# Performance work log

Hardware: AMD Instinct MI355X
Metric: run time of the kernel (lower is better)

## Reference

```python
import jax, jax.numpy as jnp
import numpy as np

GN_EPS = 1e-5
G = 8          # SKA groups
SKS3 = 27      # sks**3


def _aff(x, s, b):
    # folded BatchNorm (eval): per-channel scale + shift on NCDHW tensor
    return x * s[None, :, None, None, None] + b[None, :, None, None, None]


def _c1(x, w):
    # 1x1x1 conv as channel GEMM; w: [O, I]
    return jnp.einsum('bcdhw,oc->bodhw', x, w)


def _dw5(x, w):
    # depthwise 5x5x5 conv, pad=2; w: [C, 1, 5, 5, 5]
    return jax.lax.conv_general_dilated(
        x, w, window_strides=(1, 1, 1), padding=[(2, 2)] * 3,
        dimension_numbers=('NCDHW', 'OIDHW', 'NCDHW'),
        feature_group_count=x.shape[1])


def setup_inputs() -> dict:
    key = jax.random.key(0)
    ks = jax.random.split(key, 24)
    B, C, D, H, W = 2, 64, 32, 32, 32

    def n(k, shape, scale=1.0):
        return jax.random.normal(k, shape, jnp.float32) * scale

    def u(k, shape):
        return jax.random.uniform(k, shape, jnp.float32, 0.5, 1.5)

    return {
        'x': n(ks[0], (B, C, D, H, W)),
        'w1': n(ks[1], (32, 64), 64 ** -0.5),
        's1': u(ks[2], (32,)), 'b1': n(ks[3], (32,), 0.1),
        'w2': n(ks[4], (32, 1, 5, 5, 5), 125 ** -0.5),
        's2': u(ks[5], (32,)), 'b2': n(ks[6], (32,), 0.1),
        'w3': n(ks[7], (32, 32), 32 ** -0.5),
        's3': u(ks[8], (32,)), 'b3': n(ks[9], (32,), 0.1),
        'w4': n(ks[10], (216, 32), 32 ** -0.5), 'b4': n(ks[11], (216,), 0.1),
        'gn_g': u(ks[12], (216,)), 'gn_b': n(ks[13], (216,), 0.1),
        'bn_s': u(ks[14], (64,)), 'bn_b': n(ks[15], (64,), 0.1),
        'pw1_w': n(ks[16], (128, 64), 64 ** -0.5),
        'pw1_s': u(ks[17], (128,)), 'pw1_b': n(ks[18], (128,), 0.1),
        'pw2_w': n(ks[19], (64, 128), 128 ** -0.5),
        'pw2_s': u(ks[20], (64,)), 'pw2_b': n(ks[21], (64,), 0.1),
    }


def reference(x, w1, s1, b1, w2, s2, b2, w3, s3, b3, w4, b4,
              gn_g, gn_b, bn_s, bn_b,
              pw1_w, pw1_s, pw1_b, pw2_w, pw2_s, pw2_b):
    B, C, D, H, W = x.shape

    # ---- LKP3D: dynamic kernel generation ----
    a = jax.nn.relu(_aff(_c1(x, w1), s1, b1))          # cv1 + BN + ReLU
    a = _aff(_dw5(a, w2), s2, b2)                      # cv2 (5^3 dw) + BN
    a = jax.nn.relu(_aff(_c1(a, w3), s3, b3))          # cv3 + BN + ReLU
    wk = _c1(a, w4) + b4[None, :, None, None, None]    # cv4: [B,216,D,H,W]
    # GroupNorm: num_groups = dim//groups = 8, channels = 216
    g = wk.reshape(B, G, SKS3, D, H, W)
    mu = g.mean(axis=(2, 3, 4, 5), keepdims=True)
    var = g.var(axis=(2, 3, 4, 5), keepdims=True)
    g = (g - mu) * jax.lax.rsqrt(var + GN_EPS)
    wk = g.reshape(B, G * SKS3, D, H, W) * gn_g[None, :, None, None, None] \
         + gn_b[None, :, None, None, None]
    wk = wk.reshape(B, G, SKS3, D, H, W)               # [B, G, 27, D, H, W]

    # ---- SKA3D: apply dynamic kernels (27 shifted copies, grouped) ----
    offs = [(di, hi, wi) for di in (-1, 0, 1) for hi in (-1, 0, 1) for wi in (-1, 0, 1)]
    patches = jnp.stack(
        [jnp.roll(x, (-di, -hi, -wi), axis=(2, 3, 4)) for di, hi, wi in offs],
        axis=2)                                        # [B, C, 27, D, H, W]
    p = patches.reshape(B, G, C // G, SKS3, D, H, W)
    sk = jnp.einsum('bgckdhw,bgkdhw->bgcdhw', p, wk).reshape(B, C, D, H, W)

    y = _aff(sk, bn_s, bn_b) + x                       # LSConv BN + residual

    # ---- FFN (residual): pw1 + BN + ReLU + pw2 + BN ----
    f = jax.nn.relu(_aff(_c1(y, pw1_w), pw1_s, pw1_b))
    f = _aff(_c1(f, pw2_w), pw2_s, pw2_b)
    return y + f
```

## Files before the change

### kernel.cpp

```cpp
#include <hip/hip_runtime.h>

#define SPAT 32768
#define BATCH 2
#define GN_EPS 1e-5f

__device__ __forceinline__ void fma2(float2& a, const float2& v, float w) {
    a.x = fmaf(v.x, w, a.x); a.y = fmaf(v.y, w, a.y);
}

template <int CIN, int NO, bool RELU, bool AFF>
__global__ __launch_bounds__(256) void k_c1(
    const float* __restrict__ in, const float* __restrict__ w,
    const float* __restrict__ sc, const float* __restrict__ bi,
    float* __restrict__ out, int Cout)
{
    int q = blockIdx.x * 256 + threadIdx.x;
    int o0 = blockIdx.y * NO, b = blockIdx.z;
    const float2* ip = (const float2*)(in + (size_t)b * CIN * SPAT) + q;
    float2 acc[NO];
#pragma unroll
    for (int i = 0; i < NO; ++i) acc[i] = {0.f, 0.f};
#pragma unroll 4
    for (int c = 0; c < CIN; ++c) {
        float2 v = ip[(size_t)c * (SPAT / 2)];
#pragma unroll
        for (int i = 0; i < NO; ++i)
            fma2(acc[i], v, w[(o0 + i) * CIN + c]);
    }
    float2* op = (float2*)(out + (size_t)b * Cout * SPAT) + q;
#pragma unroll
    for (int i = 0; i < NO; ++i) {
        int o = o0 + i;
        float scale = AFF ? sc[o] : 1.f;
        float shift = bi[o];
        float2 r = acc[i];
        r.x = r.x * scale + shift; r.y = r.y * scale + shift;
        if (RELU) { r.x = fmaxf(r.x, 0.f); r.y = fmaxf(r.y, 0.f); }
        op[(size_t)o * (SPAT / 2)] = r;
    }
}

__global__ __launch_bounds__(256) void k_gram(
    const float* __restrict__ a, float* __restrict__ partial)
{
    __shared__ float lds[32 * 257];
    int blk = blockIdx.x, b = blockIdx.z;
    const float* ap = a + (size_t)b * 32 * SPAT + blk * 256;
    for (int i = threadIdx.x; i < 32 * 64; i += 256) {
        int m = i >> 6, p4 = (i & 63) * 4;
        float4 v = *(const float4*)(ap + (size_t)m * SPAT + p4);
        lds[m * 257 + p4 + 0] = v.x; lds[m * 257 + p4 + 1] = v.y;
        lds[m * 257 + p4 + 2] = v.z; lds[m * 257 + p4 + 3] = v.w;
    }
    __syncthreads();
    float* outp = partial + (size_t)(b * 128 + blk) * 1056;
#pragma unroll
    for (int it = 0; it < 4; ++it) {
        int pid = threadIdx.x + it * 256;
        const float* pa = &lds[(pid >> 5) * 257];
        const float* pb = &lds[(pid & 31) * 257];
        float acc = 0.f;
#pragma unroll 8
        for (int p = 0; p < 256; ++p) acc = fmaf(pa[p], pb[p], acc);
        outp[pid] = acc;
    }
    if (threadIdx.x < 32) {
        const float* pa = &lds[threadIdx.x * 257];
        float scc = 0.f;
#pragma unroll 8
        for (int p = 0; p < 256; ++p) scc += pa[p];
        outp[1024 + threadIdx.x] = scc;
    }
}

__global__ __launch_bounds__(512) void k_stats(
    const float* __restrict__ partial, const float* __restrict__ w4,
    const float* __restrict__ b4, float* __restrict__ stats)
{
    __shared__ float G[2 * 1056];
    __shared__ float sred[432], ssred[432];
    for (int e = threadIdx.x; e < 2 * 1056; e += 512) {
        int b = e / 1056, pid = e % 1056;
        float acc = 0.f;
#pragma unroll 8
        for (int blk = 0; blk < 128; ++blk)
            acc += partial[(size_t)(b * 128 + blk) * 1056 + pid];
        G[e] = acc;
    }
    __syncthreads();
    if (threadIdx.x < 432) {
        int t = threadIdx.x;
        int b = t / 216, r = t % 216, g = r / 27, k = r % 27;
        const float* wk = w4 + (g * 27 + k) * 32;
        float wreg[32];
#pragma unroll
        for (int m = 0; m < 32; ++m) wreg[m] = wk[m];
        const float* Gb = &G[b * 1056];
        const float* Sb = &G[b * 1056 + 1024];
        float sk = 0.f, ssk = 0.f;
#pragma unroll
        for (int m = 0; m < 32; ++m) {
            sk = fmaf(wreg[m], Sb[m], sk);
            float dot = 0.f;
#pragma unroll
            for (int mm = 0; mm < 32; ++mm)
                dot = fmaf(wreg[mm], Gb[m * 32 + mm], dot);
            ssk = fmaf(wreg[m], dot, ssk);
        }
        float bb = b4[g * 27 + k];
        float NN = (float)SPAT;
        ssk += 2.f * bb * sk + NN * bb * bb;
        sk  += NN * bb;
        sred[t] = sk; ssred[t] = ssk;
    }
    __syncthreads();
    if (threadIdx.x < 16) {
        int bg = threadIdx.x;
        float s = 0.f, ss = 0.f;
        for (int k = 0; k < 27; ++k) { s += sred[bg * 27 + k]; ss += ssred[bg * 27 + k]; }
        float N27 = 27.f * (float)SPAT;
        float mu = s / N27;
        float var = ss / N27 - mu * mu;
        stats[bg * 2 + 0] = mu;
        stats[bg * 2 + 1] = rsqrtf(var + GN_EPS);
    }
}

__global__ __launch_bounds__(256) void k_ska(
    const float* __restrict__ x, const float* __restrict__ wk,
    const float* __restrict__ stats,
    const float* __restrict__ gn_g, const float* __restrict__ gn_b,
    const float* __restrict__ bn_s, const float* __restrict__ bn_b,
    float* __restrict__ y)
{
    int q = blockIdx.x * 256 + threadIdx.x;
    int s = q * 4;
    int g = blockIdx.y, b = blockIdx.z;
    int bg = b * 8 + g;
    float mu  = stats[bg * 2 + 0];
    float inv = stats[bg * 2 + 1];
    int d = s >> 10, h = (s >> 5) & 31, w0 = s & 31;
    int lane = threadIdx.x & 63;
    int xl_src = (lane & 56) | ((lane + 7) & 7);
    int xr_src = (lane & 56) | ((lane + 1) & 7);
    const float* xg = x + ((size_t)(b * 64 + g * 8)) * SPAT;
    const float* wp = wk + ((size_t)(b * 216 + g * 27)) * SPAT + s;

    float4 acc[8];
    float4 xc[8];
#pragma unroll
    for (int c = 0; c < 8; ++c) acc[c] = {0.f, 0.f, 0.f, 0.f};

#pragma unroll
    for (int kd = 0; kd < 3; ++kd) {
        int zd = (d + kd + 31) & 31;
#pragma unroll
        for (int kh = 0; kh < 3; ++kh) {
            int zh = (h + kh + 31) & 31;
            int kbase = (kd * 3 + kh) * 3;
            float wn[3][4];
#pragma unroll
            for (int kw = 0; kw < 3; ++kw) {
                int kk = kbase + kw;
                float4 wq = *(const float4*)(wp + (size_t)kk * SPAT);
                float A = gn_g[g * 27 + kk] * inv;
                float B = gn_b[g * 27 + kk] - mu * A;
                wn[kw][0] = wq.x * A + B;
                wn[kw][1] = wq.y * A + B;
                wn[kw][2] = wq.z * A + B;
                wn[kw][3] = wq.w * A + B;
            }
            int rowoff = zd * 1024 + zh * 32;
            bool center = (kd == 1) && (kh == 1);
#pragma unroll
            for (int c = 0; c < 8; ++c) {
                float4 m = *(const float4*)(xg + (size_t)c * SPAT + rowoff + w0);
                if (center) xc[c] = m;
                float xl = __shfl(m.w, xl_src, 64);
                float xr = __shfl(m.x, xr_src, 64);
                float win[6] = {xl, m.x, m.y, m.z, m.w, xr};
#pragma unroll
                for (int kw = 0; kw < 3; ++kw) {
                    acc[c].x = fmaf(win[0 + kw], wn[kw][0], acc[c].x);
                    acc[c].y = fmaf(win[1 + kw], wn[kw][1], acc[c].y);
                    acc[c].z = fmaf(win[2 + kw], wn[kw][2], acc[c].z);
                    acc[c].w = fmaf(win[3 + kw], wn[kw][3], acc[c].w);
                }
            }
        }
    }
#pragma unroll
    for (int c = 0; c < 8; ++c) {
        int ch = g * 8 + c;
        float bs = bn_s[ch], bb = bn_b[ch];
        float4 r;
        r.x = acc[c].x * bs + bb + xc[c].x;
        r.y = acc[c].y * bs + bb + xc[c].y;
        r.z = acc[c].z * bs + bb + xc[c].z;
        r.w = acc[c].w * bs + bb + xc[c].w;
        *(float4*)(y + ((size_t)(b * 64 + ch)) * SPAT + s) = r;
    }
}

__global__ __launch_bounds__(256, 4) void k_dw5(
    const float* __restrict__ in, const float* __restrict__ w2,
    const float* __restrict__ s2, const float* __restrict__ b2,
    float* __restrict__ out)
{
    __shared__ float lds[6 * 36 * 40];
    int tid = threadIdx.x;
    int d0 = blockIdx.x * 2;
    int c = blockIdx.y, b = blockIdx.z;
    const float* ip = in + ((size_t)(b * 32 + c)) * SPAT;

    float4 z = {0.f, 0.f, 0.f, 0.f};
    for (int i = tid; i < 6 * 36 * 40 / 4; i += 256)
        ((float4*)lds)[i] = z;
    __syncthreads();
    for (int i = tid; i < 6 * 256; i += 256) {
        int p = i >> 8, rem = i & 255;
        int r = rem >> 3, c4 = (rem & 7) * 4;
        int d = d0 - 2 + p;
        if (d >= 0 && d < 32) {
            float4 v = *(const float4*)(ip + d * 1024 + r * 32 + c4);
            *(float4*)&lds[p * 1440 + (r + 2) * 40 + (c4 + 4)] = v;
        }
    }
    __syncthreads();

    float scl = s2[c], shf = b2[c];
    const float* wt = w2 + c * 125;
#pragma unroll
    for (int k = 0; k < 2; ++k) {
        int j = tid + k * 256;
        int pd = j >> 8, rem = j & 255;
        int hr = rem >> 3, w4i = (rem & 7) * 4;
        float4 acc = {0.f, 0.f, 0.f, 0.f};
#pragma unroll
        for (int kd = 0; kd < 5; ++kd) {
            const float* pl = &lds[(pd + kd) * 1440];
#pragma unroll
            for (int kh = 0; kh < 5; ++kh) {
                const float* row = pl + (hr + kh) * 40 + w4i;
                float4 r0 = *(const float4*)(row);
                float4 r1 = *(const float4*)(row + 4);
                float4 r2 = *(const float4*)(row + 8);
                float win[12] = {r0.x, r0.y, r0.z, r0.w,
                                 r1.x, r1.y, r1.z, r1.w,
                                 r2.x, r2.y, r2.z, r2.w};
#pragma unroll
                for (int kw = 0; kw < 5; ++kw) {
                    float wv = wt[kd * 25 + kh * 5 + kw];
                    acc.x = fmaf(wv, win[2 + 0 + kw], acc.x);
                    acc.y = fmaf(wv, win[2 + 1 + kw], acc.y);
                    acc.z = fmaf(wv, win[2 + 2 + kw], acc.z);
                    acc.w = fmaf(wv, win[2 + 3 + kw], acc.w);
                }
            }
        }
        acc.x = acc.x * scl + shf; acc.y = acc.y * scl + shf;
        acc.z = acc.z * scl + shf; acc.w = acc.w * scl + shf;
        *(float4*)(out + ((size_t)(b * 32 + c)) * SPAT
                   + (d0 + pd) * 1024 + hr * 32 + w4i) = acc;
    }
}

template <int NO>
__global__ __launch_bounds__(256) void k_pw2_out(
    const float* __restrict__ f1, const float* __restrict__ w,
    const float* __restrict__ sc, const float* __restrict__ bi,
    const float* __restrict__ yres, float* __restrict__ out)
{
    int q = blockIdx.x * 256 + threadIdx.x;
    int o0 = blockIdx.y * NO, b = blockIdx.z;
    const float2* ip = (const float2*)(f1 + (size_t)b * 128 * SPAT) + q;
    float2 acc[NO];
#pragma unroll
    for (int i = 0; i < NO; ++i) acc[i] = {0.f, 0.f};
#pragma unroll 4
    for (int c = 0; c < 128; ++c) {
        float2 v = ip[(size_t)c * (SPAT / 2)];
#pragma unroll
        for (int i = 0; i < NO; ++i)
            fma2(acc[i], v, w[(o0 + i) * 128 + c]);
    }
    const float2* yp = (const float2*)(yres + (size_t)b * 64 * SPAT) + q;
    float2* op = (float2*)(out + (size_t)b * 64 * SPAT) + q;
#pragma unroll
    for (int i = 0; i < NO; ++i) {
        int o = o0 + i;
        float scale = sc[o], shift = bi[o];
        float2 yv = yp[(size_t)o * (SPAT / 2)];
        float2 r = acc[i];
        r.x = r.x * scale + shift + yv.x;
        r.y = r.y * scale + shift + yv.y;
        op[(size_t)o * (SPAT / 2)] = r;
    }
}

extern "C" void kernel_launch(void* const* d_in, const int* in_sizes, int n_in,
                              void* d_out, int out_size, void* d_ws, size_t ws_size,
                              hipStream_t stream)
{
    const float* x     = (const float*)d_in[0];
    const float* w1    = (const float*)d_in[1];
    const float* s1    = (const float*)d_in[2];
    const float* b1    = (const float*)d_in[3];
    const float* w2    = (const float*)d_in[4];
    const float* s2    = (const float*)d_in[5];
    const float* b2    = (const float*)d_in[6];
    const float* w3    = (const float*)d_in[7];
    const float* s3    = (const float*)d_in[8];
    const float* b3    = (const float*)d_in[9];
    const float* w4    = (const float*)d_in[10];
    const float* b4    = (const float*)d_in[11];
    const float* gn_g  = (const float*)d_in[12];
    const float* gn_b  = (const float*)d_in[13];
    const float* bn_s  = (const float*)d_in[14];
    const float* bn_b  = (const float*)d_in[15];
    const float* pw1_w = (const float*)d_in[16];
    const float* pw1_s = (const float*)d_in[17];
    const float* pw1_b = (const float*)d_in[18];
    const float* pw2_w = (const float*)d_in[19];
    const float* pw2_s = (const float*)d_in[20];
    const float* pw2_b = (const float*)d_in[21];

    float* ws    = (float*)d_ws;
    float* a1    = ws;
    float* a2    = a1 + (size_t)BATCH * 32 * SPAT;
    float* yb    = ws;
    float* wkb   = ws + (size_t)BATCH * 64 * SPAT;
    float* f1    = wkb;
    float* part  = wkb + (size_t)BATCH * 216 * SPAT;
    float* stats = part + (size_t)256 * 1056;

    dim3 blk(256);
    k_c1<64, 8, true, true><<<dim3(SPAT / 512, 4, BATCH), blk, 0, stream>>>(
        x, w1, s1, b1, a1, 32);
    k_dw5<<<dim3(16, 32, BATCH), blk, 0, stream>>>(a1, w2, s2, b2, a2);
    k_c1<32, 8, true, true><<<dim3(SPAT / 512, 4, BATCH), blk, 0, stream>>>(
        a2, w3, s3, b3, a1, 32);
    k_gram<<<dim3(128, 1, BATCH), blk, 0, stream>>>(a1, part);
    k_stats<<<dim3(1), dim3(512), 0, stream>>>(part, w4, b4, stats);
    k_c1<32, 8, false, false><<<dim3(SPAT / 512, 27, BATCH), blk, 0, stream>>>(
        a1, w4, nullptr, b4, wkb, 216);
    k_ska<<<dim3(SPAT / 1024, 8, BATCH), blk, 0, stream>>>(
        x, wkb, stats, gn_g, gn_b, bn_s, bn_b, yb);
    k_c1<64, 8, true, true><<<dim3(SPAT / 512, 16, BATCH), blk, 0, stream>>>(
        yb, pw1_w, pw1_s, pw1_b, f1, 128);
    k_pw2_out<8><<<dim3(SPAT / 512, 8, BATCH), blk, 0, stream>>>(
        f1, pw2_w, pw2_s, pw2_b, yb, (float*)d_out);
}
```

Baseline: 281.3 us.

## Fuse FFN into one kernel and compute all output channels per thread

```diff
diff --git a/kernel.cpp b/kernel.cpp
--- a/kernel.cpp
+++ b/kernel.cpp
@@ -4,40 +4,99 @@
 #define BATCH 2
 #define GN_EPS 1e-5f
 
-__device__ __forceinline__ void fma2(float2& a, const float2& v, float w) {
-    a.x = fmaf(v.x, w, a.x); a.y = fmaf(v.y, w, a.y);
-}
-
-template <int CIN, int NO, bool RELU, bool AFF>
-__global__ __launch_bounds__(256) void k_c1(
+template <int CIN, int COUT, bool RELU>
+__global__ __launch_bounds__(256) void k_rc1(
     const float* __restrict__ in, const float* __restrict__ w,
     const float* __restrict__ sc, const float* __restrict__ bi,
-    float* __restrict__ out, int Cout)
-{
-    int q = blockIdx.x * 256 + threadIdx.x;
-    int o0 = blockIdx.y * NO, b = blockIdx.z;
-    const float2* ip = (const float2*)(in + (size_t)b * CIN * SPAT) + q;
-    float2 acc[NO];
-#pragma unroll
-    for (int i = 0; i < NO; ++i) acc[i] = {0.f, 0.f};
+    float* __restrict__ out)
+{
+    int pos = blockIdx.x * 256 + threadIdx.x;
+    int b = blockIdx.z;
+    const float* ip = in + (size_t)b * CIN * SPAT + pos;
+    float acc[COUT];
+#pragma unroll
+    for (int o = 0; o < COUT; ++o) acc[o] = 0.f;
 #pragma unroll 4
     for (int c = 0; c < CIN; ++c) {
-        float2 v = ip[(size_t)c * (SPAT / 2)];
-#pragma unroll
-        for (int i = 0; i < NO; ++i)
-            fma2(acc[i], v, w[(o0 + i) * CIN + c]);
-    }
-    float2* op = (float2*)(out + (size_t)b * Cout * SPAT) + q;
-#pragma unroll
-    for (int i = 0; i < NO; ++i) {
-        int o = o0 + i;
-        float scale = AFF ? sc[o] : 1.f;
-        float shift = bi[o];
-        float2 r = acc[i];
-        r.x = r.x * scale + shift; r.y = r.y * scale + shift;
-        if (RELU) { r.x = fmaxf(r.x, 0.f); r.y = fmaxf(r.y, 0.f); }
-        op[(size_t)o * (SPAT / 2)] = r;
-    }
+        float v = ip[(size_t)c * SPAT];
+#pragma unroll
+        for (int o = 0; o < COUT; ++o)
+            acc[o] = fmaf(v, w[o * CIN + c], acc[o]);
+    }
+    float* op = out + (size_t)b * COUT * SPAT + pos;
+#pragma unroll
+    for (int o = 0; o < COUT; ++o) {
+        float r = acc[o] * sc[o] + bi[o];
+        if (RELU) r = fmaxf(r, 0.f);
+        op[(size_t)o * SPAT] = r;
+    }
+}
+
+__global__ __launch_bounds__(256) void k_cv4r(
+    const float* __restrict__ a, const float* __restrict__ w4,
+    const float* __restrict__ b4, float* __restrict__ wk)
+{
+    int pos = blockIdx.x * 256 + threadIdx.x;
+    int o0 = blockIdx.y * 54, b = blockIdx.z;
+    const float* ip = a + (size_t)b * 32 * SPAT + pos;
+    float acc[54];
+#pragma unroll
+    for (int j = 0; j < 54; ++j) acc[j] = 0.f;
+#pragma unroll 4
+    for (int c = 0; c < 32; ++c) {
+        float v = ip[(size_t)c * SPAT];
+#pragma unroll
+        for (int j = 0; j < 54; ++j)
+            acc[j] = fmaf(v, w4[(o0 + j) * 32 + c], acc[j]);
+    }
+    float* op = wk + ((size_t)b * 216 + o0) * SPAT + pos;
+#pragma unroll
+    for (int j = 0; j < 54; ++j)
+        op[(size_t)j * SPAT] = acc[j] + b4[o0 + j];
+}
+
+__global__ __launch_bounds__(256) void k_ffn(
+    const float* __restrict__ yin,
+    const float* __restrict__ w1v, const float* __restrict__ s1v,
+    const float* __restrict__ b1v,
+    const float* __restrict__ w2v, const float* __restrict__ s2v,
+    const float* __restrict__ b2v,
+    float* __restrict__ out)
+{
+    int pos = blockIdx.x * 256 + threadIdx.x;
+    int b = blockIdx.z;
+    const float* ip = yin + (size_t)b * 64 * SPAT + pos;
+    float y[64];
+#pragma unroll
+    for (int c = 0; c < 64; ++c) y[c] = ip[(size_t)c * SPAT];
+    float acc[64];
+#pragma unroll
+    for (int o = 0; o < 64; ++o) acc[o] = 0.f;
+#pragma unroll 1
+    for (int fc0 = 0; fc0 < 128; fc0 += 16) {
+        float f[16];
+#pragma unroll
+        for (int j = 0; j < 16; ++j) {
+            float a = 0.f;
+#pragma unroll
+            for (int c = 0; c < 64; ++c)
+                a = fmaf(y[c], w1v[(fc0 + j) * 64 + c], a);
+            a = a * s1v[fc0 + j] + b1v[fc0 + j];
+            f[j] = fmaxf(a, 0.f);
+        }
+#pragma unroll
+        for (int o = 0; o < 64; ++o) {
+            float a = acc[o];
+#pragma unroll
+            for (int j = 0; j < 16; ++j)
+                a = fmaf(f[j], w2v[o * 128 + fc0 + j], a);
+            acc[o] = a;
+        }
+    }
+    float* op = out + (size_t)b * 64 * SPAT + pos;
+#pragma unroll
+    for (int o = 0; o < 64; ++o)
+        op[(size_t)o * SPAT] = acc[o] * s2v[o] + b2v[o] + y[o];
 }
 
 __global__ __launch_bounds__(256) void k_gram(
@@ -202,22 +261,22 @@
     }
 }
 
-__global__ __launch_bounds__(256, 4) void k_dw5(
+__global__ __launch_bounds__(256) void k_dw5(
     const float* __restrict__ in, const float* __restrict__ w2,
     const float* __restrict__ s2, const float* __restrict__ b2,
     float* __restrict__ out)
 {
-    __shared__ float lds[6 * 36 * 40];
+    __shared__ float lds[8 * 36 * 40];
     int tid = threadIdx.x;
-    int d0 = blockIdx.x * 2;
+    int d0 = blockIdx.x * 4;
     int c = blockIdx.y, b = blockIdx.z;
     const float* ip = in + ((size_t)(b * 32 + c)) * SPAT;
 
     float4 z = {0.f, 0.f, 0.f, 0.f};
-    for (int i = tid; i < 6 * 36 * 40 / 4; i += 256)
+    for (int i = tid; i < 8 * 36 * 40 / 4; i += 256)
         ((float4*)lds)[i] = z;
     __syncthreads();
-    for (int i = tid; i < 6 * 256; i += 256) {
+    for (int i = tid; i < 8 * 256; i += 256) {
         int p = i >> 8, rem = i & 255;
         int r = rem >> 3, c4 = (rem & 7) * 4;
         int d = d0 - 2 + p;
@@ -231,7 +290,7 @@
     float scl = s2[c], shf = b2[c];
     const float* wt = w2 + c * 125;
 #pragma unroll
-    for (int k = 0; k < 2; ++k) {
+    for (int k = 0; k < 4; ++k) {
         int j = tid + k * 256;
         int pd = j >> 8, rem = j & 255;
         int hr = rem >> 3, w4i = (rem & 7) * 4;
@@ -262,39 +321,6 @@
         acc.z = acc.z * scl + shf; acc.w = acc.w * scl + shf;
         *(float4*)(out + ((size_t)(b * 32 + c)) * SPAT
                    + (d0 + pd) * 1024 + hr * 32 + w4i) = acc;
-    }
-}
-
-template <int NO>
-__global__ __launch_bounds__(256) void k_pw2_out(
-    const float* __restrict__ f1, const float* __restrict__ w,
-    const float* __restrict__ sc, const float* __restrict__ bi,
-    const float* __restrict__ yres, float* __restrict__ out)
-{
-    int q = blockIdx.x * 256 + threadIdx.x;
-    int o0 = blockIdx.y * NO, b = blockIdx.z;
-    const float2* ip = (const float2*)(f1 + (size_t)b * 128 * SPAT) + q;
-    float2 acc[NO];
-#pragma unroll
-    for (int i = 0; i < NO; ++i) acc[i] = {0.f, 0.f};
-#pragma unroll 4
-    for (int c = 0; c < 128; ++c) {
-        float2 v = ip[(size_t)c * (SPAT / 2)];
-#pragma unroll
-        for (int i = 0; i < NO; ++i)
-            fma2(acc[i], v, w[(o0 + i) * 128 + c]);
-    }
-    const float2* yp = (const float2*)(yres + (size_t)b * 64 * SPAT) + q;
-    float2* op = (float2*)(out + (size_t)b * 64 * SPAT) + q;
-#pragma unroll
-    for (int i = 0; i < NO; ++i) {
-        int o = o0 + i;
-        float scale = sc[o], shift = bi[o];
-        float2 yv = yp[(size_t)o * (SPAT / 2)];
-        float2 r = acc[i];
-        r.x = r.x * scale + shift + yv.x;
-        r.y = r.y * scale + shift + yv.y;
-        op[(size_t)o * (SPAT / 2)] = r;
     }
 }
 
@@ -330,24 +356,21 @@
     float* a2    = a1 + (size_t)BATCH * 32 * SPAT;
     float* yb    = ws;
     float* wkb   = ws + (size_t)BATCH * 64 * SPAT;
-    float* f1    = wkb;
     float* part  = wkb + (size_t)BATCH * 216 * SPAT;
     float* stats = part + (size_t)256 * 1056;
 
     dim3 blk(256);
-    k_c1<64, 8, true, true><<<dim3(SPAT / 512, 4, BATCH), blk, 0, stream>>>(
-        x, w1, s1, b1, a1, 32);
-    k_dw5<<<dim3(16, 32, BATCH), blk, 0, stream>>>(a1, w2, s2, b2, a2);
-    k_c1<32, 8, true, true><<<dim3(SPAT / 512, 4, BATCH), blk, 0, stream>>>(
-        a2, w3, s3, b3, a1, 32);
+    k_rc1<64, 32, true><<<dim3(SPAT / 256, 1, BATCH), blk, 0, stream>>>(
+        x, w1, s1, b1, a1);
+    k_dw5<<<dim3(8, 32, BATCH), blk, 0, stream>>>(a1, w2, s2, b2, a2);
+    k_rc1<32, 32, true><<<dim3(SPAT / 256, 1, BATCH), blk, 0, stream>>>(
+        a2, w3, s3, b3, a1);
     k_gram<<<dim3(128, 1, BATCH), blk, 0, stream>>>(a1, part);
     k_stats<<<dim3(1), dim3(512), 0, stream>>>(part, w4, b4, stats);
-    k_c1<32, 8, false, false><<<dim3(SPAT / 512, 27, BATCH), blk, 0, stream>>>(
-        a1, w4, nullptr, b4, wkb, 216);
+    k_cv4r<<<dim3(SPAT / 256, 4, BATCH), blk, 0, stream>>>(
+        a1, w4, b4, wkb);
     k_ska<<<dim3(SPAT / 1024, 8, BATCH), blk, 0, stream>>>(
         x, wkb, stats, gn_g, gn_b, bn_s, bn_b, yb);
-    k_c1<64, 8, true, true><<<dim3(SPAT / 512, 16, BATCH), blk, 0, stream>>>(
-        yb, pw1_w, pw1_s, pw1_b, f1, 128);
-    k_pw2_out<8><<<dim3(SPAT / 512, 8, BATCH), blk, 0, stream>>>(
-        f1, pw2_w, pw2_s, pw2_b, yb, (float*)d_out);
-}
+    k_ffn<<<dim3(SPAT / 256, 1, BATCH), blk, 0, stream>>>(
+        yb, pw1_w, pw1_s, pw1_b, pw2_w, pw2_s, pw2_b, (float*)d_out);
+}
```

New measurement: 542.6 us. 92.9% more time.
